# Optimization experiments

Measured on AMD Instinct MI355X. Metric: run time of the kernel, lower is better.

Reference implementation:

```python
import jax, jax.numpy as jnp
import numpy as np

B, T, C = 2, 2048, 4096
NH, NKV, HD = 32, 8, 128
GROUPS = NH // NKV
THETA = 10000.0


def _rope_tables(seq_len, dim, theta, dtype):
    inv_freq = 1.0 / (theta ** (jnp.arange(0, dim, 2, dtype=jnp.float32) / dim))
    t = jnp.arange(seq_len, dtype=jnp.float32)
    freqs = jnp.outer(t, inv_freq)            # [T, dim/2]
    emb = jnp.concatenate([freqs, freqs], -1)  # [T, dim]
    return jnp.cos(emb).astype(dtype), jnp.sin(emb).astype(dtype)


def _rotate_half(x):
    h = x.shape[-1] // 2
    return jnp.concatenate([-x[..., h:], x[..., :h]], axis=-1)


def setup_inputs() -> dict:
    key = jax.random.key(0)
    ks = jax.random.split(key, 5)
    s = 1.0 / np.sqrt(C)
    return {
        "x": jax.random.normal(ks[0], (B, T, C), jnp.float32),
        "wq": jax.random.normal(ks[1], (C, NH * HD), jnp.float32) * s,
        "wk": jax.random.normal(ks[2], (C, NKV * HD), jnp.float32) * s,
        "wv": jax.random.normal(ks[3], (C, NKV * HD), jnp.float32) * s,
        "wo": jax.random.normal(ks[4], (NH * HD, C), jnp.float32) * s,
    }


def reference(x, wq, wk, wv, wo):
    b, t, c = x.shape
    q = (x @ wq).reshape(b, t, NH, HD).transpose(0, 2, 1, 3)    # [B,NH,T,HD]
    k = (x @ wk).reshape(b, t, NKV, HD).transpose(0, 2, 1, 3)   # [B,NKV,T,HD]
    v = (x @ wv).reshape(b, t, NKV, HD).transpose(0, 2, 1, 3)
    cos, sin = _rope_tables(t, HD, THETA, x.dtype)              # [T,HD]
    cos = cos[None, None]
    sin = sin[None, None]
    q = q * cos + _rotate_half(q) * sin
    k = k * cos + _rotate_half(k) * sin
    # GQA: broadcast KV heads over groups via einsum instead of materializing repeat
    qg = q.reshape(b, NKV, GROUPS, t, HD)
    scores = jnp.einsum('bkgqd,bkld->bkgql', qg, k) * (HD ** -0.5)  # [B,NKV,G,T,T]
    causal = jnp.triu(jnp.full((t, t), -jnp.inf, dtype=x.dtype), k=1)
    scores = scores + causal
    attn = jax.nn.softmax(scores, axis=-1)
    out = jnp.einsum('bkgql,bkld->bkgqd', attn, v)              # [B,NKV,G,T,HD]
    out = out.reshape(b, NH, t, HD).transpose(0, 2, 1, 3).reshape(b, t, NH * HD)
    return out @ wo
```

## Files before the change

### kernel.cpp

```cpp
#include <hip/hip_runtime.h>
#include <hip/hip_bf16.h>
#include <math.h>

#define B_ 2
#define T_ 2048
#define C_ 4096
#define NH_ 32
#define NKV_ 8
#define HD_ 128
#define M_ (B_*T_)
#define QKVN_ (NH_*HD_ + 2*NKV_*HD_)

using bf16 = __hip_bfloat16;
typedef __bf16 bf16x8 __attribute__((ext_vector_type(8)));
typedef float f32x4 __attribute__((ext_vector_type(4)));

__device__ inline f32x4 mfma16(bf16x8 a, bf16x8 b, f32x4 c) {
    return __builtin_amdgcn_mfma_f32_16x16x32_bf16(a, b, c, 0, 0, 0);
}

__global__ __launch_bounds__(256) void cast_f32_bf16(const float* __restrict__ in,
                                                     bf16* __restrict__ out, int n4) {
    int i = blockIdx.x * 256 + threadIdx.x;
    if (i >= n4) return;
    float4 v = reinterpret_cast<const float4*>(in)[i];
    union { bf16 h[4]; uint2 u; } o;
    o.h[0] = __float2bfloat16(v.x);
    o.h[1] = __float2bfloat16(v.y);
    o.h[2] = __float2bfloat16(v.z);
    o.h[3] = __float2bfloat16(v.w);
    reinterpret_cast<uint2*>(out)[i] = o.u;
}

__global__ __launch_bounds__(256) void transpose_cast(const float* __restrict__ in,
                                                      bf16* __restrict__ out, int K, int N) {
    __shared__ float tile[32][33];
    int tx = threadIdx.x & 31, ty = threadIdx.x >> 5;
    int n0 = blockIdx.x << 5, k0 = blockIdx.y << 5;
#pragma unroll
    for (int p = 0; p < 4; ++p)
        tile[p*8 + ty][tx] = in[(size_t)(k0 + p*8 + ty) * N + n0 + tx];
    __syncthreads();
#pragma unroll
    for (int p = 0; p < 4; ++p)
        out[(size_t)(n0 + p*8 + ty) * K + k0 + tx] = __float2bfloat16(tile[tx][p*8 + ty]);
}

__device__ inline void store_out(float* p, float v) { *p = v; }
__device__ inline void store_out(bf16*  p, float v) { *p = __float2bfloat16(v); }

template <typename OutT>
__global__ __launch_bounds__(512, 2) void gemm256(const bf16* __restrict__ A,
                                                  const bf16* __restrict__ Bt,
                                                  OutT* __restrict__ C,
                                                  int M, int N, int K) {
    __shared__ __align__(16) char lds[131072];
    const int tid = threadIdx.x;
    const int wid = tid >> 6, lane = tid & 63;
    const int lq = lane & 15, lg = lane >> 4;
    const int wrow = wid >> 2, wcol = wid & 3;

    const int nwg = gridDim.x;
    const int q8 = nwg >> 3;
    const int wg = (blockIdx.x & 7) * q8 + (blockIdx.x >> 3);
    const int nby = M >> 8;
    const int by = wg % nby, bx = wg / nby;
    const int brow = by << 8, bcol = bx << 8;

    const bf16* Ag = A + (size_t)brow * K;
    const bf16* Bg = Bt + (size_t)bcol * K;
    const int nt = K >> 6;

    const int srow = (wid << 3) + (lane >> 3);
    const int schunk = (lane & 7) ^ ((lane >> 3) & 7);

#define STAGE_MAT(gbase, ldsoff, t2, cbuf)                                              \
    {                                                                                   \
        _Pragma("unroll")                                                               \
        for (int h = 0; h < 2; ++h)                                                     \
            _Pragma("unroll")                                                           \
            for (int l = 0; l < 2; ++l) {                                               \
                const int r0 = h * 128 + l * 64;                                        \
                const char* src = (const char*)(gbase) +                                \
                    ((size_t)(r0 + srow) * K + (size_t)(t2) * 64) * 2 + schunk * 16;    \
                char* dst = &lds[(ldsoff) + (cbuf) * 32768 + (r0 + (wid << 3)) * 128];  \
                __builtin_amdgcn_global_load_lds(                                       \
                    (const __attribute__((address_space(1))) void*)src,                 \
                    (__attribute__((address_space(3))) void*)dst, 16, 0, 0);            \
            }                                                                           \
    }

#define LDA(cbuf, mh, mf, ks) \
    (*(const bf16x8*)&lds[(cbuf)*32768 + (wrow*128 + (mh)*64 + (mf)*16 + lq)*128 + ((((ks)*4 + lg)) ^ (lq & 7))*16])
#define LDB(cbuf, nh, nf, ks) \
    (*(const bf16x8*)&lds[65536 + (cbuf)*32768 + (wcol*64 + (nh)*32 + (nf)*16 + lq)*128 + ((((ks)*4 + lg)) ^ (lq & 7))*16])

    f32x4 acc[8][4] = {};
    bf16x8 a[4][2], b0[2][2], b1[2][2];

    STAGE_MAT(Ag, 0,     0, 0); STAGE_MAT(Bg, 65536, 0, 0);
    STAGE_MAT(Ag, 0,     1, 1); STAGE_MAT(Bg, 65536, 1, 1);
    asm volatile("s_waitcnt vmcnt(8)" ::: "memory");
    __builtin_amdgcn_s_barrier();

    for (int t = 0; t < nt; ++t) {
        const int cb = t & 1;
        const bool more = (t + 2) < nt;

#pragma unroll
        for (int mf = 0; mf < 4; ++mf) { a[mf][0] = LDA(cb, 0, mf, 0); a[mf][1] = LDA(cb, 0, mf, 1); }
#pragma unroll
        for (int nf = 0; nf < 2; ++nf) { b0[nf][0] = LDB(cb, 0, nf, 0); b0[nf][1] = LDB(cb, 0, nf, 1); }
        __builtin_amdgcn_s_barrier();
        __builtin_amdgcn_s_setprio(1);
#pragma unroll
        for (int mf = 0; mf < 4; ++mf)
#pragma unroll
            for (int nf = 0; nf < 2; ++nf)
#pragma unroll
                for (int ks = 0; ks < 2; ++ks)
                    acc[mf][nf] = mfma16(a[mf][ks], b0[nf][ks], acc[mf][nf]);
        __builtin_amdgcn_s_setprio(0);
        asm volatile("s_waitcnt lgkmcnt(0)" ::: "memory");
        __builtin_amdgcn_s_barrier();

#pragma unroll
        for (int nf = 0; nf < 2; ++nf) { b1[nf][0] = LDB(cb, 1, nf, 0); b1[nf][1] = LDB(cb, 1, nf, 1); }
        __builtin_amdgcn_s_barrier();
        __builtin_amdgcn_s_setprio(1);
#pragma unroll
        for (int mf = 0; mf < 4; ++mf)
#pragma unroll
            for (int nf = 0; nf < 2; ++nf)
#pragma unroll
                for (int ks = 0; ks < 2; ++ks)
                    acc[mf][2 + nf] = mfma16(a[mf][ks], b1[nf][ks], acc[mf][2 + nf]);
        __builtin_amdgcn_s_setprio(0);
        asm volatile("s_waitcnt lgkmcnt(0)" ::: "memory");
        __builtin_amdgcn_s_barrier();

#pragma unroll
        for (int mf = 0; mf < 4; ++mf) { a[mf][0] = LDA(cb, 1, mf, 0); a[mf][1] = LDA(cb, 1, mf, 1); }
        if (more) STAGE_MAT(Bg, 65536, t + 2, cb);
        __builtin_amdgcn_s_barrier();
        __builtin_amdgcn_s_setprio(1);
#pragma unroll
        for (int mf = 0; mf < 4; ++mf)
#pragma unroll
            for (int nf = 0; nf < 2; ++nf)
#pragma unroll
                for (int ks = 0; ks < 2; ++ks)
                    acc[4 + mf][2 + nf] = mfma16(a[mf][ks], b1[nf][ks], acc[4 + mf][2 + nf]);
        __builtin_amdgcn_s_setprio(0);
        asm volatile("s_waitcnt lgkmcnt(0)" ::: "memory");
        __builtin_amdgcn_s_barrier();

        if (more) STAGE_MAT(Ag, 0, t + 2, cb);
        __builtin_amdgcn_s_barrier();
        __builtin_amdgcn_s_setprio(1);
#pragma unroll
        for (int mf = 0; mf < 4; ++mf)
#pragma unroll
            for (int nf = 0; nf < 2; ++nf)
#pragma unroll
                for (int ks = 0; ks < 2; ++ks)
                    acc[4 + mf][nf] = mfma16(a[mf][ks], b0[nf][ks], acc[4 + mf][nf]);
        __builtin_amdgcn_s_setprio(0);
        if (t < nt - 1) {
            if (t == nt - 2) asm volatile("s_waitcnt vmcnt(0) lgkmcnt(0)" ::: "memory");
            else             asm volatile("s_waitcnt vmcnt(8) lgkmcnt(0)" ::: "memory");
            __builtin_amdgcn_s_barrier();
        }
    }
#undef STAGE_MAT
#undef LDA
#undef LDB

#pragma unroll
    for (int mf = 0; mf < 8; ++mf)
#pragma unroll
        for (int nf = 0; nf < 4; ++nf)
#pragma unroll
            for (int r = 0; r < 4; ++r) {
                int row = brow + wrow * 128 + mf * 16 + lg * 4 + r;
                int col = bcol + wcol * 64 + nf * 16 + lq;
                store_out(&C[(size_t)row * N + col], acc[mf][nf][r]);
            }
}

__global__ __launch_bounds__(256) void rope_qk(const bf16* __restrict__ qkv,
                                               bf16* __restrict__ outp,
                                               int nheads, int col_off, float qscale) {
    size_t idx = (size_t)blockIdx.x * 256 + threadIdx.x;
    int i = (int)(idx & 63);
    size_t rest = idx >> 6;
    int t = (int)(rest % T_);
    rest /= T_;
    int hh = (int)(rest % nheads);
    int b = (int)(rest / nheads);

    const bf16* src = qkv + (size_t)(b * T_ + t) * QKVN_ + col_off + hh * HD_;
    float x0 = __bfloat162float(src[i]);
    float x1 = __bfloat162float(src[i + 64]);
    float inv = exp2f((float)i * -0.20762050593045952f);
    float th = (float)t * inv;
    float s = sinf(th), c = cosf(th);
    bf16* dst = outp + ((size_t)(b * nheads + hh) * T_ + t) * HD_;
    dst[i]      = __float2bfloat16((x0 * c - x1 * s) * qscale);
    dst[i + 64] = __float2bfloat16((x1 * c + x0 * s) * qscale);
}

__global__ __launch_bounds__(256) void vtrans(const bf16* __restrict__ qkv,
                                              bf16* __restrict__ vt) {
    __shared__ bf16 tile[32][33];
    int gx = blockIdx.x;
    int dt = gx & 3;
    int tt = (gx >> 2) & 63;
    int kv = (gx >> 8) & 7;
    int b  = gx >> 11;
    int d0 = dt * 32, t0 = tt * 32;
    int tx = threadIdx.x & 31, ty = threadIdx.x >> 5;

    const bf16* src = qkv + (size_t)(b * T_ + t0) * QKVN_ + (NH_*HD_ + NKV_*HD_) + kv * HD_ + d0;
#pragma unroll
    for (int p = 0; p < 4; ++p)
        tile[p*8 + ty][tx] = src[(size_t)(p*8 + ty) * QKVN_ + tx];
    __syncthreads();
    bf16* dst = vt + ((size_t)((b * NKV_ + kv) * HD_ + d0)) * T_ + t0;
#pragma unroll
    for (int p = 0; p < 4; ++p)
        dst[(size_t)(p*8 + ty) * T_ + tx] = tile[tx][p*8 + ty];
}

__global__ __launch_bounds__(512) void fattn(const bf16* __restrict__ Q,
                                             const bf16* __restrict__ Kt,
                                             const bf16* __restrict__ VT,
                                             bf16* __restrict__ O) {
    const int lin = blockIdx.x;
    const int kv = lin & 7;
    const int b  = (lin >> 3) & 1;
    const int idx = lin >> 4;
    const int h  = kv * 4 + (idx & 3);
    const int jp = idx >> 2;

    const int tid = threadIdx.x, wid = tid >> 6, lane = tid & 63;
    const int lq = lane & 15, lg = lane >> 4;

    const bf16* Kp = Kt + (size_t)(b * NKV_ + kv) * T_ * HD_;
    const bf16* Vp = VT + (size_t)(b * NKV_ + kv) * HD_ * T_;

    __shared__ __align__(16) bf16 Ks[2][64][128];
    __shared__ __align__(16) bf16 Vs[2][128][64];
    __shared__ __align__(16) bf16 p_lds[8][32][72];

    const float THR_L2 = 11.5416f;

#define STAGE_KV(cbuf, tt)                                                           \
    { _Pragma("unroll") for (int j = 0; j < 2; ++j) {                                \
        int kidx = j * 64 + lane;                                                    \
        int krow = wid * 8 + (kidx >> 4);                                            \
        int kch  = (kidx & 15) ^ (krow & 15);                                        \
        const bf16* ksrc = Kp + (size_t)((tt) * 64 + krow) * HD_ + kch * 8;          \
        __builtin_amdgcn_global_load_lds(                                            \
            (const __attribute__((address_space(1))) void*)ksrc,                     \
            (__attribute__((address_space(3))) void*)&Ks[cbuf][wid*8 + j*4][0],      \
            16, 0, 0);                                                               \
      }                                                                              \
      _Pragma("unroll") for (int j = 0; j < 2; ++j) {                                \
        int vidx = j * 64 + lane;                                                    \
        int vrow = wid * 16 + (vidx >> 3);                                           \
        int vch  = (vidx & 7) ^ (vrow & 7);                                          \
        const bf16* vsrc = Vp + (size_t)vrow * T_ + (tt) * 64 + vch * 8;             \
        __builtin_amdgcn_global_load_lds(                                            \
            (const __attribute__((address_space(1))) void*)vsrc,                     \
            (__attribute__((address_space(3))) void*)&Vs[cbuf][wid*16 + j*8][0],     \
            16, 0, 0);                                                               \
      } }

    for (int half = 0; half < 2; ++half) {
        const int qt = half ? (7 - jp) : jp;
        const int q0 = qt * 256 + wid * 32;
        const int kv_end = q0 + 32;
        const int NT = qt * 4 + 4;

        const bf16* Qp = Q + ((size_t)(b * NH_ + h) * T_ + q0) * HD_;
        bf16x8 qf[2][4];
#pragma unroll
        for (int m = 0; m < 2; ++m)
#pragma unroll
            for (int c = 0; c < 4; ++c)
                qf[m][c] = *(const bf16x8*)&Qp[(size_t)(m*16 + lq) * HD_ + c * 32 + lg * 8];

        f32x4 oacc[2][8] = {};
        float m_r[2] = {-INFINITY, -INFINITY};
        float l_r[2] = {0.f, 0.f};

        STAGE_KV(0, 0);
        STAGE_KV(1, 1);
        asm volatile("s_waitcnt vmcnt(4)" ::: "memory");
        __builtin_amdgcn_s_barrier();

        for (int t = 0; t < NT; ++t) {
            const int cb = t & 1;
            const int t0 = t * 64;

            if (t0 < kv_end) {
                f32x4 st[2][4] = {};
#pragma unroll
                for (int n = 0; n < 4; ++n) {
                    bf16x8 kf[4];
#pragma unroll
                    for (int c = 0; c < 4; ++c)
                        kf[c] = *(const bf16x8*)((const char*)&Ks[cb][n*16 + lq][0]
                                                  + (((c*4 + lg) ^ lq) << 4));
                    __builtin_amdgcn_s_setprio(1);
#pragma unroll
                    for (int c = 0; c < 4; ++c) {
                        st[0][n] = mfma16(kf[c], qf[0][c], st[0][n]);
                        st[1][n] = mfma16(kf[c], qf[1][c], st[1][n]);
                    }
                    __builtin_amdgcn_s_setprio(0);
                }

#pragma unroll
                for (int m = 0; m < 2; ++m) {
                    const int qq = q0 + m*16 + lq;
#pragma unroll
                    for (int n = 0; n < 4; ++n)
#pragma unroll
                        for (int r = 0; r < 4; ++r) {
                            int kk = t0 + n*16 + lg*4 + r;
                            if (kk > qq) st[m][n][r] = -INFINITY;
                        }
                }

                float rmax[2];
#pragma unroll
                for (int m = 0; m < 2; ++m) {
                    float v = st[m][0][0];
#pragma unroll
                    for (int n = 0; n < 4; ++n)
#pragma unroll
                        for (int r = 0; r < 4; ++r) v = fmaxf(v, st[m][n][r]);
                    v = fmaxf(v, __shfl_xor(v, 16));
                    v = fmaxf(v, __shfl_xor(v, 32));
                    rmax[m] = v;
                }

                float dmax = fmaxf(rmax[0] - m_r[0], rmax[1] - m_r[1]);
                if (__any(dmax > THR_L2)) {
#pragma unroll
                    for (int m = 0; m < 2; ++m) {
                        float mnew = fmaxf(m_r[m], rmax[m]);
                        float alpha = exp2f(m_r[m] - mnew);
                        m_r[m] = mnew;
                        l_r[m] *= alpha;
#pragma unroll
                        for (int r = 0; r < 4; ++r) {
                            float a_pv = __shfl(alpha, lg*4 + r);
#pragma unroll
                            for (int f = 0; f < 8; ++f) oacc[m][f][r] *= a_pv;
                        }
                    }
                }

#pragma unroll
                for (int m = 0; m < 2; ++m) {
                    float rsum = 0.f;
#pragma unroll
                    for (int n = 0; n < 4; ++n)
#pragma unroll
                        for (int r = 0; r < 4; ++r) {
                            float p = exp2f(st[m][n][r] - m_r[m]);
                            st[m][n][r] = p;
                            rsum += p;
                        }
                    rsum += __shfl_xor(rsum, 16);
                    rsum += __shfl_xor(rsum, 32);
                    l_r[m] += rsum;
                }

#pragma unroll
                for (int m = 0; m < 2; ++m)
#pragma unroll
                    for (int n = 0; n < 4; ++n) {
                        union { bf16 hh[4]; uint2 u; } pk;
#pragma unroll
                        for (int r = 0; r < 4; ++r) pk.hh[r] = __float2bfloat16(st[m][n][r]);
                        *(uint2*)&p_lds[wid][m*16 + lq][n*16 + lg*4] = pk.u;
                    }

#pragma unroll
                for (int ks = 0; ks < 2; ++ks) {
                    bf16x8 pa0 = *(const bf16x8*)&p_lds[wid][lq]     [ks*32 + lg*8];
                    bf16x8 pa1 = *(const bf16x8*)&p_lds[wid][16 + lq][ks*32 + lg*8];
                    bf16x8 vf[8];
#pragma unroll
                    for (int f = 0; f < 8; ++f)
                        vf[f] = *(const bf16x8*)((const char*)&Vs[cb][f*16 + lq][0]
                                                  + (((ks*4 + lg) ^ (lq & 7)) << 4));
                    __builtin_amdgcn_s_setprio(1);
#pragma unroll
                    for (int f = 0; f < 8; ++f) {
                        oacc[0][f] = mfma16(pa0, vf[f], oacc[0][f]);
                        oacc[1][f] = mfma16(pa1, vf[f], oacc[1][f]);
                    }
                    __builtin_amdgcn_s_setprio(0);
                }
            }

            __builtin_amdgcn_s_barrier();
            if (t + 2 < NT) {
                STAGE_KV(cb, t + 2);
                asm volatile("s_waitcnt vmcnt(4)" ::: "memory");
            } else {
                asm volatile("s_waitcnt vmcnt(0)" ::: "memory");
            }
            __builtin_amdgcn_s_barrier();
        }

#pragma unroll
        for (int m = 0; m < 2; ++m) {
            float rinv = __builtin_amdgcn_rcpf(l_r[m]);
#pragma unroll
            for (int r = 0; r < 4; ++r) {
                float rl = __shfl(rinv, lg*4 + r);
                int row = q0 + m*16 + lg*4 + r;
#pragma unroll
                for (int f = 0; f < 8; ++f) {
                    int d = f*16 + lq;
                    O[((size_t)(b * T_ + row) * NH_ + h) * HD_ + d] =
                        __float2bfloat16(oacc[m][f][r] * rl);
                }
            }
        }
    }
#undef STAGE_KV
}

extern "C" void kernel_launch(void* const* d_in, const int* in_sizes, int n_in,
                              void* d_out, int out_size, void* d_ws, size_t ws_size,
                              hipStream_t stream) {
    const float* x  = (const float*)d_in[0];
    const float* wq = (const float*)d_in[1];
    const float* wk = (const float*)d_in[2];
    const float* wv = (const float*)d_in[3];
    const float* wo = (const float*)d_in[4];
    float* out = (float*)d_out;

    bf16* ws    = (bf16*)d_ws;
    bf16* xb    = ws;
    bf16* wqkvT = xb + (size_t)M_ * C_;
    bf16* woT   = wqkvT + (size_t)QKVN_ * C_;
    bf16* qkv   = woT + (size_t)C_ * C_;

    bf16* attn = xb;
    bf16* q_r  = wqkvT;
    bf16* k_r  = q_r + (size_t)B_ * NH_ * T_ * HD_;
    bf16* vt   = k_r + (size_t)B_ * NKV_ * T_ * HD_;

    cast_f32_bf16<<<(M_ * C_ / 4 + 255) / 256, 256, 0, stream>>>(x, xb, M_ * C_ / 4);
    transpose_cast<<<dim3(128, 128), 256, 0, stream>>>(wq, wqkvT, C_, NH_ * HD_);
    transpose_cast<<<dim3(32, 128), 256, 0, stream>>>(wk, wqkvT + (size_t)(NH_ * HD_) * C_, C_, NKV_ * HD_);
    transpose_cast<<<dim3(32, 128), 256, 0, stream>>>(wv, wqkvT + (size_t)(NH_ * HD_ + NKV_ * HD_) * C_, C_, NKV_ * HD_);
    transpose_cast<<<dim3(128, 128), 256, 0, stream>>>(wo, woT, NH_ * HD_, C_);

    gemm256<bf16><<<dim3((QKVN_ / 256) * (M_ / 256)), 512, 0, stream>>>(xb, wqkvT, qkv, M_, QKVN_, C_);

    rope_qk<<<(B_ * NH_ * T_ * 64) / 256, 256, 0, stream>>>(qkv, q_r, NH_, 0, 0.12751741230963214f);
    rope_qk<<<(B_ * NKV_ * T_ * 64) / 256, 256, 0, stream>>>(qkv, k_r, NKV_, NH_ * HD_, 1.0f);
    vtrans<<<B_ * NKV_ * (T_ / 32) * (HD_ / 32), 256, 0, stream>>>(qkv, vt);

    fattn<<<dim3(256), 512, 0, stream>>>(q_r, k_r, vt, attn);

    gemm256<float><<<dim3((C_ / 256) * (M_ / 256)), 512, 0, stream>>>(attn, woT, out, M_, C_, C_);
}
```

Baseline: 561.5 us.

## Split GEMM tile staging into half-loads interleaved across MFMA phases

Restructures the bf16 GEMM main loop into a two-step unrolled schedule. Global-to-LDS loads are issued in half-tile pieces spread across the four MFMA phases instead of whole matrices at once. Loads run a different distance ahead for A and B, and the waitcnt thresholds are reduced. The goal is to keep the memory pipeline busy more evenly and hide load latency behind MFMA work. The cost is a fragile prefetch and barrier ordering, and the loop now assumes nt is even.

```diff
diff --git a/kernel.cpp b/kernel.cpp
--- a/kernel.cpp
+++ b/kernel.cpp
@@ -74,20 +74,18 @@
     const int srow = (wid << 3) + (lane >> 3);
     const int schunk = (lane & 7) ^ ((lane >> 3) & 7);
 
-#define STAGE_MAT(gbase, ldsoff, t2, cbuf)                                              \
+#define STAGE_HALF(gbase, ldsoff, t2, cbuf, hf)                                         \
     {                                                                                   \
         _Pragma("unroll")                                                               \
-        for (int h = 0; h < 2; ++h)                                                     \
-            _Pragma("unroll")                                                           \
-            for (int l = 0; l < 2; ++l) {                                               \
-                const int r0 = h * 128 + l * 64;                                        \
-                const char* src = (const char*)(gbase) +                                \
-                    ((size_t)(r0 + srow) * K + (size_t)(t2) * 64) * 2 + schunk * 16;    \
-                char* dst = &lds[(ldsoff) + (cbuf) * 32768 + (r0 + (wid << 3)) * 128];  \
-                __builtin_amdgcn_global_load_lds(                                       \
-                    (const __attribute__((address_space(1))) void*)src,                 \
-                    (__attribute__((address_space(3))) void*)dst, 16, 0, 0);            \
-            }                                                                           \
+        for (int l = 0; l < 2; ++l) {                                                   \
+            const int r0 = (hf) * 128 + l * 64;                                         \
+            const char* src = (const char*)(gbase) +                                    \
+                ((size_t)(r0 + srow) * K + (size_t)(t2) * 64) * 2 + schunk * 16;        \
+            char* dst = &lds[(ldsoff) + (cbuf) * 32768 + (r0 + (wid << 3)) * 128];      \
+            __builtin_amdgcn_global_load_lds(                                           \
+                (const __attribute__((address_space(1))) void*)src,                     \
+                (__attribute__((address_space(3))) void*)dst, 16, 0, 0);                \
+        }                                                                               \
     }
 
 #define LDA(cbuf, mh, mf, ks) \
@@ -95,86 +93,76 @@
 #define LDB(cbuf, nh, nf, ks) \
     (*(const bf16x8*)&lds[65536 + (cbuf)*32768 + (wcol*64 + (nh)*32 + (nf)*16 + lq)*128 + ((((ks)*4 + lg)) ^ (lq & 7))*16])
 
+#define READ_A(cbuf, mh) \
+    { _Pragma("unroll") for (int mf = 0; mf < 4; ++mf) { a[mf][0] = LDA(cbuf, mh, mf, 0); a[mf][1] = LDA(cbuf, mh, mf, 1); } }
+#define READ_B(cbuf, nh, breg) \
+    { _Pragma("unroll") for (int nf = 0; nf < 2; ++nf) { breg[nf][0] = LDB(cbuf, nh, nf, 0); breg[nf][1] = LDB(cbuf, nh, nf, 1); } }
+#define MFMA_Q(am, an, breg)                                                     \
+    { __builtin_amdgcn_s_setprio(1);                                             \
+      _Pragma("unroll") for (int mf = 0; mf < 4; ++mf)                           \
+          _Pragma("unroll") for (int nf = 0; nf < 2; ++nf)                       \
+              _Pragma("unroll") for (int ks = 0; ks < 2; ++ks)                   \
+                  acc[(am) + mf][(an) + nf] = mfma16(a[mf][ks], breg[nf][ks],    \
+                                                     acc[(am) + mf][(an) + nf]); \
+      __builtin_amdgcn_s_setprio(0); }
+#define BAR() __builtin_amdgcn_s_barrier()
+
     f32x4 acc[8][4] = {};
     bf16x8 a[4][2], b0[2][2], b1[2][2];
 
-    STAGE_MAT(Ag, 0,     0, 0); STAGE_MAT(Bg, 65536, 0, 0);
-    STAGE_MAT(Ag, 0,     1, 1); STAGE_MAT(Bg, 65536, 1, 1);
-    asm volatile("s_waitcnt vmcnt(8)" ::: "memory");
-    __builtin_amdgcn_s_barrier();
-
-    for (int t = 0; t < nt; ++t) {
-        const int cb = t & 1;
-        const bool more = (t + 2) < nt;
-
-#pragma unroll
-        for (int mf = 0; mf < 4; ++mf) { a[mf][0] = LDA(cb, 0, mf, 0); a[mf][1] = LDA(cb, 0, mf, 1); }
-#pragma unroll
-        for (int nf = 0; nf < 2; ++nf) { b0[nf][0] = LDB(cb, 0, nf, 0); b0[nf][1] = LDB(cb, 0, nf, 1); }
-        __builtin_amdgcn_s_barrier();
-        __builtin_amdgcn_s_setprio(1);
-#pragma unroll
-        for (int mf = 0; mf < 4; ++mf)
-#pragma unroll
-            for (int nf = 0; nf < 2; ++nf)
-#pragma unroll
-                for (int ks = 0; ks < 2; ++ks)
-                    acc[mf][nf] = mfma16(a[mf][ks], b0[nf][ks], acc[mf][nf]);
-        __builtin_amdgcn_s_setprio(0);
-        asm volatile("s_waitcnt lgkmcnt(0)" ::: "memory");
-        __builtin_amdgcn_s_barrier();
-
-#pragma unroll
-        for (int nf = 0; nf < 2; ++nf) { b1[nf][0] = LDB(cb, 1, nf, 0); b1[nf][1] = LDB(cb, 1, nf, 1); }
-        __builtin_amdgcn_s_barrier();
-        __builtin_amdgcn_s_setprio(1);
-#pragma unroll
-        for (int mf = 0; mf < 4; ++mf)
-#pragma unroll
-            for (int nf = 0; nf < 2; ++nf)
-#pragma unroll
-                for (int ks = 0; ks < 2; ++ks)
-                    acc[mf][2 + nf] = mfma16(a[mf][ks], b1[nf][ks], acc[mf][2 + nf]);
-        __builtin_amdgcn_s_setprio(0);
-        asm volatile("s_waitcnt lgkmcnt(0)" ::: "memory");
-        __builtin_amdgcn_s_barrier();
-
-#pragma unroll
-        for (int mf = 0; mf < 4; ++mf) { a[mf][0] = LDA(cb, 1, mf, 0); a[mf][1] = LDA(cb, 1, mf, 1); }
-        if (more) STAGE_MAT(Bg, 65536, t + 2, cb);
-        __builtin_amdgcn_s_barrier();
-        __builtin_amdgcn_s_setprio(1);
-#pragma unroll
-        for (int mf = 0; mf < 4; ++mf)
-#pragma unroll
-            for (int nf = 0; nf < 2; ++nf)
-#pragma unroll
-                for (int ks = 0; ks < 2; ++ks)
-                    acc[4 + mf][2 + nf] = mfma16(a[mf][ks], b1[nf][ks], acc[4 + mf][2 + nf]);
-        __builtin_amdgcn_s_setprio(0);
-        asm volatile("s_waitcnt lgkmcnt(0)" ::: "memory");
-        __builtin_amdgcn_s_barrier();
-
-        if (more) STAGE_MAT(Ag, 0, t + 2, cb);
-        __builtin_amdgcn_s_barrier();
-        __builtin_amdgcn_s_setprio(1);
-#pragma unroll
-        for (int mf = 0; mf < 4; ++mf)
-#pragma unroll
-            for (int nf = 0; nf < 2; ++nf)
-#pragma unroll
-                for (int ks = 0; ks < 2; ++ks)
-                    acc[4 + mf][nf] = mfma16(a[mf][ks], b0[nf][ks], acc[4 + mf][nf]);
-        __builtin_amdgcn_s_setprio(0);
-        if (t < nt - 1) {
-            if (t == nt - 2) asm volatile("s_waitcnt vmcnt(0) lgkmcnt(0)" ::: "memory");
-            else             asm volatile("s_waitcnt vmcnt(8) lgkmcnt(0)" ::: "memory");
-            __builtin_amdgcn_s_barrier();
-        }
+    STAGE_HALF(Ag, 0,     0, 0, 0); STAGE_HALF(Ag, 0,     0, 0, 1);
+    STAGE_HALF(Bg, 65536, 0, 0, 0); STAGE_HALF(Bg, 65536, 0, 0, 1);
+    STAGE_HALF(Bg, 65536, 1, 1, 0); STAGE_HALF(Bg, 65536, 1, 1, 1);
+    asm volatile("s_waitcnt vmcnt(4)" ::: "memory");
+    BAR();
+
+    for (int i = 0; i < (nt >> 1); ++i) {
+        const int u = 2 * i;
+        const bool s_u2 = (u + 2) < nt;
+        const bool s_v2 = (u + 3) < nt;
+
+        READ_A(0, 0); READ_B(0, 0, b0);
+        STAGE_HALF(Ag, 0, u + 1, 1, 0);
+        MFMA_Q(0, 0, b0);
+        BAR();
+        READ_B(0, 1, b1);
+        STAGE_HALF(Ag, 0, u + 1, 1, 1);
+        MFMA_Q(0, 2, b1);
+        BAR();
+        READ_A(0, 1);
+        if (s_u2) STAGE_HALF(Bg, 65536, u + 2, 0, 0);
+        MFMA_Q(4, 2, b1);
+        BAR();
+        if (s_u2) STAGE_HALF(Bg, 65536, u + 2, 0, 1);
+        MFMA_Q(4, 0, b0);
+        if (s_u2) asm volatile("s_waitcnt vmcnt(4)" ::: "memory");
+        else      asm volatile("s_waitcnt vmcnt(0)" ::: "memory");
+        BAR();
+        READ_A(1, 0); READ_B(1, 0, b0);
+        if (s_u2) STAGE_HALF(Ag, 0, u + 2, 0, 0);
+        MFMA_Q(0, 0, b0);
+        BAR();
+        READ_B(1, 1, b1);
+        if (s_u2) STAGE_HALF(Ag, 0, u + 2, 0, 1);
+        MFMA_Q(0, 2, b1);
+        BAR();
+        READ_A(1, 1);
+        if (s_v2) STAGE_HALF(Bg, 65536, u + 3, 1, 0);
+        MFMA_Q(4, 2, b1);
+        BAR();
+        if (s_v2) STAGE_HALF(Bg, 65536, u + 3, 1, 1);
+        MFMA_Q(4, 0, b0);
+        if (s_v2) asm volatile("s_waitcnt vmcnt(4)" ::: "memory");
+        else      asm volatile("s_waitcnt vmcnt(0)" ::: "memory");
+        BAR();
     }
-#undef STAGE_MAT
+#undef STAGE_HALF
 #undef LDA
 #undef LDB
+#undef READ_A
+#undef READ_B
+#undef MFMA_Q
+#undef BAR
 
 #pragma unroll
     for (int mf = 0; mf < 8; ++mf)
```

New measurement: 527.0 us. -6.1%, faster.
